# Kernel tuning notes

Hardware: AMD Instinct MI355X
Metric: run time of the kernel (lower is better)

The kernel has to match this reference:

```python
import jax, jax.numpy as jnp
import numpy as np

B, IN, H = 4096, 1024, 1024


def setup_inputs() -> dict:
    key = jax.random.key(0)
    ks = jax.random.split(key, 16)
    s_in = 1.0 / np.sqrt(IN)
    s_h = 1.0 / np.sqrt(H)
    d = {
        "x_t": jax.random.normal(ks[0], (B, IN), jnp.float32),
        "h_prev": jax.random.normal(ks[1], (B, H), jnp.float32),
        "c_prev": jax.random.normal(ks[2], (B, H), jnp.float32),
    }
    # input->hidden weights (with bias), stored torch-style as (out, in)
    for i, name in enumerate(["ii", "if", "ig", "io"]):
        d[f"W_{name}"] = jax.random.uniform(ks[3 + i], (H, IN), jnp.float32, -s_in, s_in)
        d[f"b_{name}"] = jax.random.uniform(ks[7 + i], (H,), jnp.float32, -s_in, s_in)
    # hidden->hidden weights (no bias)
    for i, name in enumerate(["hi", "hf", "hg", "ho"]):
        d[f"W_{name}"] = jax.random.uniform(ks[11 + i], (H, H), jnp.float32, -s_h, s_h)
    return d


def reference(x_t, h_prev, c_prev,
              W_ii, b_ii, W_if, b_if, W_ig, b_ig, W_io, b_io,
              W_hi, W_hf, W_hg, W_ho):
    # Fuse the 8 small GEMMs into 2 concatenated GEMMs (same math).
    Wx = jnp.concatenate([W_ii, W_if, W_ig, W_io], axis=0)   # (4H, IN)
    Wh = jnp.concatenate([W_hi, W_hf, W_hg, W_ho], axis=0)   # (4H, H)
    b = jnp.concatenate([b_ii, b_if, b_ig, b_io], axis=0)    # (4H,)
    gates = x_t @ Wx.T + h_prev @ Wh.T + b                    # (B, 4H)
    zi, zf, zg, zo = jnp.split(gates, 4, axis=1)
    i_t = jax.nn.sigmoid(zi)
    f_t = jax.nn.sigmoid(zf)
    g_t = jnp.tanh(zg)
    o_t = jax.nn.sigmoid(zo)
    c_t = f_t * c_prev + i_t * g_t
    h_t = o_t * jnp.tanh(c_t)
    return (h_t, c_t, (i_t, f_t, g_t, o_t))
```

## Files before the change

### kernel.cpp

```cpp
#include <hip/hip_runtime.h>
#include <hip/hip_bf16.h>

#define B_DIM 4096
#define K_TOT 2048
#define H_DIM 1024

typedef short bf16x8 __attribute__((ext_vector_type(8)));
typedef float f32x4 __attribute__((ext_vector_type(4)));
typedef unsigned short u16x8 __attribute__((ext_vector_type(8)));

typedef __attribute__((address_space(1))) const unsigned gas_u32;
typedef __attribute__((address_space(3))) unsigned las_u32;

static __device__ __forceinline__ unsigned short f2bf(float f) {
  union { float f; unsigned u; } v; v.f = f;
  unsigned r = v.u + 0x7FFF + ((v.u >> 16) & 1);
  return (unsigned short)(r >> 16);
}

__global__ void pack_a(const float* __restrict__ x, const float* __restrict__ hp,
                       u16x8* __restrict__ A) {
  int t = blockIdx.x * blockDim.x + threadIdx.x;
  int idx = t << 3;
  int b = idx >> 11;
  int k = idx & 2047;
  const float* src = (k < 1024) ? (x + b * 1024 + k) : (hp + b * 1024 + (k - 1024));
  float4 lo = *(const float4*)src;
  float4 hi = *(const float4*)(src + 4);
  u16x8 v;
  v[0] = f2bf(lo.x); v[1] = f2bf(lo.y); v[2] = f2bf(lo.z); v[3] = f2bf(lo.w);
  v[4] = f2bf(hi.x); v[5] = f2bf(hi.y); v[6] = f2bf(hi.z); v[7] = f2bf(hi.w);
  A[t] = v;
}

__global__ void pack_w(const float* __restrict__ W0, const float* __restrict__ W1,
                       const float* __restrict__ W2, const float* __restrict__ W3,
                       const float* __restrict__ W4, const float* __restrict__ W5,
                       const float* __restrict__ W6, const float* __restrict__ W7,
                       u16x8* __restrict__ Wc) {
  int t = blockIdx.x * blockDim.x + threadIdx.x;
  int idx = t << 3;
  int n = idx >> 11;
  int k = idx & 2047;
  int gate = n >> 10;
  int j = n & 1023;
  int s = (k < 1024) ? gate : gate + 4;
  const float* base =
      (s == 0) ? W0 : (s == 1) ? W1 : (s == 2) ? W2 : (s == 3) ? W3 :
      (s == 4) ? W4 : (s == 5) ? W5 : (s == 6) ? W6 : W7;
  const float* src = base + j * 1024 + (k & 1023);
  float4 lo = *(const float4*)src;
  float4 hi = *(const float4*)(src + 4);
  u16x8 v;
  v[0] = f2bf(lo.x); v[1] = f2bf(lo.y); v[2] = f2bf(lo.z); v[3] = f2bf(lo.w);
  v[4] = f2bf(hi.x); v[5] = f2bf(hi.y); v[6] = f2bf(hi.z); v[7] = f2bf(hi.w);
  Wc[t] = v;
}

static __device__ __forceinline__ float sigm(float x) {
  return 1.0f / (1.0f + __expf(-x));
}
static __device__ __forceinline__ float tanh_fast(float x) {
  x = fminf(fmaxf(x, -15.f), 15.f);
  float t = __expf(-2.0f * x);
  return (1.0f - t) / (1.0f + t);
}

__global__ __launch_bounds__(256) void gemm_lstm(
    const unsigned short* __restrict__ A,
    const unsigned short* __restrict__ W,
    const float* __restrict__ cp,
    const float* __restrict__ bii, const float* __restrict__ bif,
    const float* __restrict__ big, const float* __restrict__ bio,
    float* __restrict__ out) {
  __shared__ unsigned short As[128 * 32];
  __shared__ unsigned short Bs[128 * 32];
  const int tid = threadIdx.x;
  const int wave = tid >> 6;
  const int lane = tid & 63;
  const int m0 = blockIdx.y << 7;
  const int j0 = blockIdx.x << 5;
  const int wm = (wave >> 1) << 6;
  const int wj16 = (wave & 1) << 4;

  f32x4 acc[4][4];
#pragma unroll
  for (int mi = 0; mi < 4; ++mi)
#pragma unroll
    for (int ni = 0; ni < 4; ++ni)
      acc[mi][ni] = (f32x4){0.f, 0.f, 0.f, 0.f};

  const int c0 = wave * 2;
  const int lr = lane >> 2;
  const int ls = lane & 3;
  const int g  = ls ^ ((lr >> 1) & 3);
  const unsigned short* aptr0 = A + (long)(m0 + c0 * 16 + lr) * K_TOT + g * 8;
  const unsigned short* aptr1 = A + (long)(m0 + (c0 + 1) * 16 + lr) * K_TOT + g * 8;
  const int rr0 = c0 * 16 + lr;
  const int rr1 = rr0 + 16;
  const unsigned short* bptr0 =
      W + (long)((rr0 >> 5) * 1024 + j0 + (rr0 & 31)) * K_TOT + g * 8;
  const unsigned short* bptr1 =
      W + (long)((rr1 >> 5) * 1024 + j0 + (rr1 & 31)) * K_TOT + g * 8;
  char* lA0 = (char*)As + c0 * 1024;
  char* lA1 = lA0 + 1024;
  char* lB0 = (char*)Bs + c0 * 1024;
  char* lB1 = lB0 + 1024;

  const int fr = lane & 15;
  const int gg = lane >> 4;
  const int sl = (gg ^ ((fr >> 1) & 3)) * 16;

  for (int k0 = 0; k0 < K_TOT; k0 += 32) {
    __builtin_amdgcn_global_load_lds((gas_u32*)(aptr0 + k0), (las_u32*)lA0, 16, 0, 0);
    __builtin_amdgcn_global_load_lds((gas_u32*)(aptr1 + k0), (las_u32*)lA1, 16, 0, 0);
    __builtin_amdgcn_global_load_lds((gas_u32*)(bptr0 + k0), (las_u32*)lB0, 16, 0, 0);
    __builtin_amdgcn_global_load_lds((gas_u32*)(bptr1 + k0), (las_u32*)lB1, 16, 0, 0);
    __syncthreads();
    bf16x8 af[4], bfv[4];
#pragma unroll
    for (int i = 0; i < 4; ++i) {
      af[i]  = *(const bf16x8*)((const char*)As + (wm + i * 16 + fr) * 64 + sl);
      bfv[i] = *(const bf16x8*)((const char*)Bs + (i * 32 + wj16 + fr) * 64 + sl);
    }
#pragma unroll
    for (int mi = 0; mi < 4; ++mi)
#pragma unroll
      for (int ni = 0; ni < 4; ++ni)
        acc[mi][ni] = __builtin_amdgcn_mfma_f32_16x16x32_bf16(af[mi], bfv[ni], acc[mi][ni], 0, 0, 0);
    __syncthreads();
  }

  const int ccol = lane & 15;
  const int crow = (lane >> 4) * 4;
  const int j = j0 + wj16 + ccol;
  const float bi = bii[j];
  const float bff = bif[j];
  const float bg = big[j];
  const float bo = bio[j];
  const long BH = (long)B_DIM * H_DIM;
#pragma unroll
  for (int mi = 0; mi < 4; ++mi) {
#pragma unroll
    for (int reg = 0; reg < 4; ++reg) {
      const int row = m0 + wm + mi * 16 + crow + reg;
      const long p = (long)row * H_DIM + j;
      const float cvp = cp[p];
      const float iv = sigm(acc[mi][0][reg] + bi);
      const float fv = sigm(acc[mi][1][reg] + bff);
      const float gv = tanh_fast(acc[mi][2][reg] + bg);
      const float ov = sigm(acc[mi][3][reg] + bo);
      const float cv = fv * cvp + iv * gv;
      const float hv = ov * tanh_fast(cv);
      out[p]          = hv;
      out[BH + p]     = cv;
      out[2 * BH + p] = iv;
      out[3 * BH + p] = fv;
      out[4 * BH + p] = gv;
      out[5 * BH + p] = ov;
    }
  }
}

extern "C" void kernel_launch(void* const* d_in, const int* in_sizes, int n_in,
                              void* d_out, int out_size, void* d_ws, size_t ws_size,
                              hipStream_t stream) {
  const float* x    = (const float*)d_in[0];
  const float* h    = (const float*)d_in[1];
  const float* c    = (const float*)d_in[2];
  const float* W_ii = (const float*)d_in[3];
  const float* b_ii = (const float*)d_in[4];
  const float* W_if = (const float*)d_in[5];
  const float* b_if = (const float*)d_in[6];
  const float* W_ig = (const float*)d_in[7];
  const float* b_ig = (const float*)d_in[8];
  const float* W_io = (const float*)d_in[9];
  const float* b_io = (const float*)d_in[10];
  const float* W_hi = (const float*)d_in[11];
  const float* W_hf = (const float*)d_in[12];
  const float* W_hg = (const float*)d_in[13];
  const float* W_ho = (const float*)d_in[14];

  unsigned short* Abf = (unsigned short*)d_ws;
  unsigned short* Wbf = (unsigned short*)((char*)d_ws + (size_t)16 * 1024 * 1024);

  pack_a<<<4096, 256, 0, stream>>>(x, h, (u16x8*)Abf);
  pack_w<<<4096, 256, 0, stream>>>(W_ii, W_if, W_ig, W_io, W_hi, W_hf, W_hg, W_ho,
                                   (u16x8*)Wbf);
  dim3 grid(H_DIM / 32, B_DIM / 128);
  gemm_lstm<<<grid, 256, 0, stream>>>(Abf, Wbf, c, b_ii, b_if, b_ig, b_io,
                                      (float*)d_out);
}
```

Measured before the change: 282.4 us.

## Double-buffer LDS tiles, merge pack kernels, use nontemporal output stores

Adds a two-stage LDS ping-pong so the next K tile's global-to-LDS loads are issued before the MFMAs on the current tile, which removes one barrier per iteration. The two bf16 pack kernels become one launch. The six fp32 output streams are written with nontemporal stores to reduce cache pollution. It doubles LDS use per block, which may lower occupancy, and overlap still depends on the compiler's waitcnt placement at the barrier.

```diff
diff --git a/kernel.cpp b/kernel.cpp
--- a/kernel.cpp
+++ b/kernel.cpp
@@ -1,5 +1,4 @@
 #include <hip/hip_runtime.h>
-#include <hip/hip_bf16.h>
 
 #define B_DIM 4096
 #define K_TOT 2048
@@ -18,43 +17,42 @@
   return (unsigned short)(r >> 16);
 }
 
-__global__ void pack_a(const float* __restrict__ x, const float* __restrict__ hp,
-                       u16x8* __restrict__ A) {
-  int t = blockIdx.x * blockDim.x + threadIdx.x;
-  int idx = t << 3;
-  int b = idx >> 11;
-  int k = idx & 2047;
-  const float* src = (k < 1024) ? (x + b * 1024 + k) : (hp + b * 1024 + (k - 1024));
+__global__ void pack_all(const float* __restrict__ x, const float* __restrict__ hp,
+                         const float* __restrict__ W0, const float* __restrict__ W1,
+                         const float* __restrict__ W2, const float* __restrict__ W3,
+                         const float* __restrict__ W4, const float* __restrict__ W5,
+                         const float* __restrict__ W6, const float* __restrict__ W7,
+                         u16x8* __restrict__ A, u16x8* __restrict__ Wc) {
+  const int t = blockIdx.x * blockDim.x + threadIdx.x;
+  const int NA = (B_DIM * K_TOT) >> 3;
+  const float* src;
+  u16x8* dst;
+  if (t < NA) {
+    int idx = t << 3;
+    int b = idx >> 11;
+    int k = idx & 2047;
+    src = (k < 1024) ? (x + b * 1024 + k) : (hp + b * 1024 + (k - 1024));
+    dst = A + t;
+  } else {
+    int u = t - NA;
+    int idx = u << 3;
+    int n = idx >> 11;
+    int k = idx & 2047;
+    int gate = n >> 10;
+    int j = n & 1023;
+    int s = (k < 1024) ? gate : gate + 4;
+    const float* base =
+        (s == 0) ? W0 : (s == 1) ? W1 : (s == 2) ? W2 : (s == 3) ? W3 :
+        (s == 4) ? W4 : (s == 5) ? W5 : (s == 6) ? W6 : W7;
+    src = base + j * 1024 + (k & 1023);
+    dst = Wc + u;
+  }
   float4 lo = *(const float4*)src;
   float4 hi = *(const float4*)(src + 4);
   u16x8 v;
   v[0] = f2bf(lo.x); v[1] = f2bf(lo.y); v[2] = f2bf(lo.z); v[3] = f2bf(lo.w);
   v[4] = f2bf(hi.x); v[5] = f2bf(hi.y); v[6] = f2bf(hi.z); v[7] = f2bf(hi.w);
-  A[t] = v;
-}
-
-__global__ void pack_w(const float* __restrict__ W0, const float* __restrict__ W1,
-                       const float* __restrict__ W2, const float* __restrict__ W3,
-                       const float* __restrict__ W4, const float* __restrict__ W5,
-                       const float* __restrict__ W6, const float* __restrict__ W7,
-                       u16x8* __restrict__ Wc) {
-  int t = blockIdx.x * blockDim.x + threadIdx.x;
-  int idx = t << 3;
-  int n = idx >> 11;
-  int k = idx & 2047;
-  int gate = n >> 10;
-  int j = n & 1023;
-  int s = (k < 1024) ? gate : gate + 4;
-  const float* base =
-      (s == 0) ? W0 : (s == 1) ? W1 : (s == 2) ? W2 : (s == 3) ? W3 :
-      (s == 4) ? W4 : (s == 5) ? W5 : (s == 6) ? W6 : W7;
-  const float* src = base + j * 1024 + (k & 1023);
-  float4 lo = *(const float4*)src;
-  float4 hi = *(const float4*)(src + 4);
-  u16x8 v;
-  v[0] = f2bf(lo.x); v[1] = f2bf(lo.y); v[2] = f2bf(lo.z); v[3] = f2bf(lo.w);
-  v[4] = f2bf(hi.x); v[5] = f2bf(hi.y); v[6] = f2bf(hi.z); v[7] = f2bf(hi.w);
-  Wc[t] = v;
+  *dst = v;
 }
 
 static __device__ __forceinline__ float sigm(float x) {
@@ -73,8 +71,8 @@
     const float* __restrict__ bii, const float* __restrict__ bif,
     const float* __restrict__ big, const float* __restrict__ bio,
     float* __restrict__ out) {
-  __shared__ unsigned short As[128 * 32];
-  __shared__ unsigned short Bs[128 * 32];
+  __shared__ unsigned short As[2][128 * 32];
+  __shared__ unsigned short Bs[2][128 * 32];
   const int tid = threadIdx.x;
   const int wave = tid >> 6;
   const int lane = tid & 63;
@@ -95,33 +93,42 @@
   const int ls = lane & 3;
   const int g  = ls ^ ((lr >> 1) & 3);
   const unsigned short* aptr0 = A + (long)(m0 + c0 * 16 + lr) * K_TOT + g * 8;
-  const unsigned short* aptr1 = A + (long)(m0 + (c0 + 1) * 16 + lr) * K_TOT + g * 8;
+  const unsigned short* aptr1 = aptr0 + 16 * K_TOT;
   const int rr0 = c0 * 16 + lr;
   const int rr1 = rr0 + 16;
   const unsigned short* bptr0 =
       W + (long)((rr0 >> 5) * 1024 + j0 + (rr0 & 31)) * K_TOT + g * 8;
   const unsigned short* bptr1 =
       W + (long)((rr1 >> 5) * 1024 + j0 + (rr1 & 31)) * K_TOT + g * 8;
-  char* lA0 = (char*)As + c0 * 1024;
-  char* lA1 = lA0 + 1024;
-  char* lB0 = (char*)Bs + c0 * 1024;
-  char* lB1 = lB0 + 1024;
+  const int stg_off = c0 * 1024;
+
+#define STAGE(buf, kk)                                                                   \
+  do {                                                                                   \
+    char* la = (char*)As + (buf) * 8192 + stg_off;                                       \
+    char* lb = (char*)Bs + (buf) * 8192 + stg_off;                                       \
+    __builtin_amdgcn_global_load_lds((gas_u32*)(aptr0 + (kk)), (las_u32*)la, 16, 0, 0);  \
+    __builtin_amdgcn_global_load_lds((gas_u32*)(aptr1 + (kk)), (las_u32*)(la + 1024), 16, 0, 0); \
+    __builtin_amdgcn_global_load_lds((gas_u32*)(bptr0 + (kk)), (las_u32*)lb, 16, 0, 0);  \
+    __builtin_amdgcn_global_load_lds((gas_u32*)(bptr1 + (kk)), (las_u32*)(lb + 1024), 16, 0, 0); \
+  } while (0)
 
   const int fr = lane & 15;
   const int gg = lane >> 4;
   const int sl = (gg ^ ((fr >> 1) & 3)) * 16;
 
+  STAGE(0, 0);
+  __syncthreads();
+
+  int cur = 0;
   for (int k0 = 0; k0 < K_TOT; k0 += 32) {
-    __builtin_amdgcn_global_load_lds((gas_u32*)(aptr0 + k0), (las_u32*)lA0, 16, 0, 0);
-    __builtin_amdgcn_global_load_lds((gas_u32*)(aptr1 + k0), (las_u32*)lA1, 16, 0, 0);
-    __builtin_amdgcn_global_load_lds((gas_u32*)(bptr0 + k0), (las_u32*)lB0, 16, 0, 0);
-    __builtin_amdgcn_global_load_lds((gas_u32*)(bptr1 + k0), (las_u32*)lB1, 16, 0, 0);
-    __syncthreads();
+    if (k0 + 32 < K_TOT) STAGE(cur ^ 1, k0 + 32);
+    const char* baseA = (const char*)As + cur * 8192;
+    const char* baseB = (const char*)Bs + cur * 8192;
     bf16x8 af[4], bfv[4];
 #pragma unroll
     for (int i = 0; i < 4; ++i) {
-      af[i]  = *(const bf16x8*)((const char*)As + (wm + i * 16 + fr) * 64 + sl);
-      bfv[i] = *(const bf16x8*)((const char*)Bs + (i * 32 + wj16 + fr) * 64 + sl);
+      af[i]  = *(const bf16x8*)(baseA + (wm + i * 16 + fr) * 64 + sl);
+      bfv[i] = *(const bf16x8*)(baseB + (i * 32 + wj16 + fr) * 64 + sl);
     }
 #pragma unroll
     for (int mi = 0; mi < 4; ++mi)
@@ -129,7 +136,9 @@
       for (int ni = 0; ni < 4; ++ni)
         acc[mi][ni] = __builtin_amdgcn_mfma_f32_16x16x32_bf16(af[mi], bfv[ni], acc[mi][ni], 0, 0, 0);
     __syncthreads();
+    cur ^= 1;
   }
+#undef STAGE
 
   const int ccol = lane & 15;
   const int crow = (lane >> 4) * 4;
@@ -152,12 +161,12 @@
       const float ov = sigm(acc[mi][3][reg] + bo);
       const float cv = fv * cvp + iv * gv;
       const float hv = ov * tanh_fast(cv);
-      out[p]          = hv;
-      out[BH + p]     = cv;
-      out[2 * BH + p] = iv;
-      out[3 * BH + p] = fv;
-      out[4 * BH + p] = gv;
-      out[5 * BH + p] = ov;
+      __builtin_nontemporal_store(hv, &out[p]);
+      __builtin_nontemporal_store(cv, &out[BH + p]);
+      __builtin_nontemporal_store(iv, &out[2 * BH + p]);
+      __builtin_nontemporal_store(fv, &out[3 * BH + p]);
+      __builtin_nontemporal_store(gv, &out[4 * BH + p]);
+      __builtin_nontemporal_store(ov, &out[5 * BH + p]);
     }
   }
 }
@@ -184,9 +193,9 @@
   unsigned short* Abf = (unsigned short*)d_ws;
   unsigned short* Wbf = (unsigned short*)((char*)d_ws + (size_t)16 * 1024 * 1024);
 
-  pack_a<<<4096, 256, 0, stream>>>(x, h, (u16x8*)Abf);
-  pack_w<<<4096, 256, 0, stream>>>(W_ii, W_if, W_ig, W_io, W_hi, W_hf, W_hg, W_ho,
-                                   (u16x8*)Wbf);
+  pack_all<<<8192, 256, 0, stream>>>(x, h, W_ii, W_if, W_ig, W_io,
+                                     W_hi, W_hf, W_hg, W_ho,
+                                     (u16x8*)Abf, (u16x8*)Wbf);
   dim3 grid(H_DIM / 32, B_DIM / 128);
   gemm_lstm<<<grid, 256, 0, stream>>>(Abf, Wbf, c, b_ii, b_if, b_ig, b_io,
                                       (float*)d_out);
```

Measured after the change: 287.6 us. Within noise of the previous version (+1.8%).
